# Kernel tuning notes

Hardware: AMD Instinct MI355X
Metric: run time of the kernel (lower is better)

## Reference

```python
import jax, jax.numpy as jnp
import numpy as np

N_SRC = 50000; N_DST = 50000; E = 800000
IN_NODE = 128; IN_EDGE = 16; OUT_NODE = 64; OUT_EDGE = 16; H = 4
LEAKY_SLOPE = 0.01  # F.leaky_relu default used inside dgl EGATConv


def setup_inputs() -> dict:
    key = jax.random.key(0)
    ks = jax.random.split(key, 11)
    return dict(
        nfeats=jax.random.normal(ks[0], (N_SRC, IN_NODE), jnp.float32),
        dst_feats=jax.random.normal(ks[1], (N_DST, IN_NODE), jnp.float32),
        reward=jax.random.uniform(ks[2], (E,), jnp.float32),
        src=jax.random.randint(ks[3], (E,), 0, N_SRC),
        dst=jax.random.randint(ks[4], (E,), 0, N_DST),
        W_ns=jax.random.normal(ks[5], (IN_NODE, H * OUT_NODE), jnp.float32) * 0.05,
        b_ns=jnp.zeros((H * OUT_NODE,), jnp.float32),
        W_ni=jax.random.normal(ks[6], (IN_NODE, H * OUT_EDGE), jnp.float32) * 0.05,
        W_nj=jax.random.normal(ks[7], (IN_NODE, H * OUT_EDGE), jnp.float32) * 0.05,
        W_fij=jax.random.normal(ks[8], (IN_EDGE, H * OUT_EDGE), jnp.float32) * 0.05,
        attn=jax.random.normal(ks[9], (H, OUT_EDGE), jnp.float32) * 0.05,
        b_e=jnp.zeros((H * OUT_EDGE,), jnp.float32),
    )


def reference(nfeats, dst_feats, reward, src, dst,
              W_ns, b_ns, W_ni, W_nj, W_fij, attn, b_e):
    # EGAT.forward with num_layers=1: efeats = reward repeated to IN_EDGE cols
    efeats = jnp.repeat(reward[:, None], IN_EDGE, axis=1)              # (E, Fe_in)
    # --- EGATConv ---
    f_ni = nfeats @ W_ni                                               # (Ns, H*Fe)
    f_nj = dst_feats @ W_nj                                            # (Nd, H*Fe)
    f_out = f_ni[src] + f_nj[dst] + efeats @ W_fij + b_e               # (E, H*Fe)
    f_out = jax.nn.leaky_relu(f_out, LEAKY_SLOPE).reshape(E, H, OUT_EDGE)
    e = jnp.einsum('ehf,hf->eh', f_out, attn)                          # (E, H)
    # edge softmax over incoming edges of each dst node (stable)
    m = jax.ops.segment_max(e, dst, num_segments=N_DST)                # (Nd, H)
    a = jnp.exp(e - m[dst])
    s = jax.ops.segment_sum(a, dst, num_segments=N_DST)                # (Nd, H)
    a = a / jnp.where(s > 0, s, 1.0)[dst]                              # (E, H)
    # weighted aggregation of projected src features
    h_src = (nfeats @ W_ns + b_ns).reshape(N_SRC, H, OUT_NODE)
    msg = h_src[src] * a[:, :, None]                                   # (E, H, Fn)
    h_out = jax.ops.segment_sum(msg, dst, num_segments=N_DST)          # (Nd, H, Fn)
    # wrapper: mean over heads then ReLU
    return jax.nn.relu(h_out.mean(axis=1))                             # (Nd, Fn)
```

## Files before the change

kernel.cpp:

```cpp
#include <hip/hip_runtime.h>

#define IN_NODE 128
#define OUT_NODE 64
#define NHEAD 4
#define HN 256
#define HE 64
#define LEAKY 0.01f

typedef __attribute__((ext_vector_type(8))) short bf16x8;
typedef __attribute__((ext_vector_type(4))) float f32x4;
typedef __attribute__((ext_vector_type(2))) float f32x2;

__device__ __forceinline__ float bf2f(unsigned short u) {
    union { unsigned u; float f; } v; v.u = ((unsigned)u) << 16; return v.f;
}
__device__ __forceinline__ unsigned short f2bf(float x) {
    union { float f; unsigned u; } v; v.f = x;
    unsigned r = v.u + 0x7FFF + ((v.u >> 16) & 1);
    return (unsigned short)(r >> 16);
}
__device__ __forceinline__ bf16x8 cvt8(float4 a, float4 b) {
    bf16x8 r;
    r[0] = (short)f2bf(a.x); r[1] = (short)f2bf(a.y);
    r[2] = (short)f2bf(a.z); r[3] = (short)f2bf(a.w);
    r[4] = (short)f2bf(b.x); r[5] = (short)f2bf(b.y);
    r[6] = (short)f2bf(b.z); r[7] = (short)f2bf(b.w);
    return r;
}
__device__ __forceinline__ f32x2 bfcvt2(unsigned d) {
    union { unsigned u; float f; } lo, hi;
    lo.u = d << 16; hi.u = d & 0xFFFF0000u;
    f32x2 r; r.x = lo.f; r.y = hi.f; return r;
}

__global__ void prep_hist(const float* __restrict__ W_fij,
                          const float* __restrict__ W_ni,
                          const float* __restrict__ W_ns,
                          const float* __restrict__ W_nj,
                          const int* __restrict__ dst,
                          float* __restrict__ wsum, unsigned short* __restrict__ WT,
                          int* __restrict__ cnt, int E) {
    int b = blockIdx.x;
    if (b == 0) {
        int k = threadIdx.x;
        if (k < 64) {
            float s = 0.f;
#pragma unroll
            for (int c = 0; c < 16; ++c) s += W_fij[c * 64 + k];
            wsum[k] = s;
        }
        return;
    }
    if (b <= 12) {
        int base = (b - 1) * 4096 + threadIdx.x;
#pragma unroll
        for (int i = 0; i < 16; ++i) {
            int idx = base + i * 256;
            int g   = idx >> 11;
            int rem = idx & 2047;
            int c   = rem >> 9;
            int l   = (rem >> 3) & 63;
            int j   = rem & 7;
            int nl  = l & 15;
            int k   = c * 32 + (l >> 4) * 8 + j;
            unsigned short v;
            if (g < 4)       v = f2bf(W_ni[k * 64  + g * 16 + nl]);
            else if (g < 20) v = f2bf(W_ns[k * 256 + (g - 4) * 16 + nl]);
            else             v = f2bf(W_nj[k * 64  + (g - 20) * 16 + nl]);
            WT[idx] = v;
        }
        return;
    }
    int i = (b - 13) * 256 + threadIdx.x;
    if (i < E) atomicAdd(&cnt[dst[i]], 1);
}

__global__ __launch_bounds__(256) void scan_all(const int* __restrict__ cnt,
                                                int* __restrict__ row_ptr,
                                                int* __restrict__ partials,
                                                int* __restrict__ flags,
                                                int n, int E, int nb) {
    __shared__ int sums[256];
    __shared__ int s_base;
    int tid = threadIdx.x, b = blockIdx.x;
    int base = b * 1024;
    int v[4]; int tsum = 0;
#pragma unroll
    for (int j = 0; j < 4; ++j) {
        int idx = base + tid * 4 + j;
        v[j] = (idx < n) ? cnt[idx] : 0;
        tsum += v[j];
    }
    sums[tid] = tsum;
    __syncthreads();
    for (int off = 1; off < 256; off <<= 1) {
        int x = (tid >= off) ? sums[tid - off] : 0;
        __syncthreads();
        sums[tid] += x;
        __syncthreads();
    }
    if (tid == 255) {
        __hip_atomic_store(&partials[b], sums[255], __ATOMIC_RELAXED, __HIP_MEMORY_SCOPE_AGENT);
        __hip_atomic_store(&flags[b], 1, __ATOMIC_RELEASE, __HIP_MEMORY_SCOPE_AGENT);
    }
    if (tid < 64) {
        int val = 0;
        if (tid < nb) {
            while (__hip_atomic_load(&flags[tid], __ATOMIC_ACQUIRE, __HIP_MEMORY_SCOPE_AGENT) == 0) {
                __builtin_amdgcn_s_sleep(1);
            }
            val = __hip_atomic_load(&partials[tid], __ATOMIC_RELAXED, __HIP_MEMORY_SCOPE_AGENT);
        }
#pragma unroll
        for (int o = 1; o < 64; o <<= 1) {
            int x = __shfl_up(val, o);
            if (tid >= o) val += x;
        }
        int off = (b > 0) ? __shfl(val, b - 1) : 0;
        if (tid == 0) s_base = off;
    }
    __syncthreads();
    int run = s_base + sums[tid] - tsum;
#pragma unroll
    for (int j = 0; j < 4; ++j) {
        int idx = base + tid * 4 + j;
        if (idx < n) row_ptr[idx] = run;
        run += v[j];
    }
    if (b == nb - 1 && tid == 0) row_ptr[n] = E;
}

template<int NG, int G0>
__device__ __forceinline__ void gemm_tile(
    const float* __restrict__ A, int rowBase, int M,
    const unsigned short* __restrict__ WB, const float* __restrict__ b_ns,
    unsigned short* __restrict__ f_ni, unsigned short* __restrict__ h_src,
    unsigned short* __restrict__ f_nj, unsigned short* As)
{
    const int t = threadIdx.x;
    const float4* A4 = reinterpret_cast<const float4*>(A);
#pragma unroll
    for (int j = 0; j < 4; ++j) {
        int gi = j * 256 + t;
        int r  = gi >> 4;
        int gr = rowBase + r; if (gr >= M) gr = M - 1;
        int fi = (gi & 15) * 2;
        float4 a0 = A4[(size_t)gr * 32 + fi];
        float4 a1 = A4[(size_t)gr * 32 + fi + 1];
        int byteoff = (gi * 16) ^ ((r & 7) << 4);
        *reinterpret_cast<bf16x8*>(reinterpret_cast<char*>(As) + byteoff) = cvt8(a0, a1);
    }
    __syncthreads();

    const int lane = t & 63, w = t >> 6;
    const int rw = rowBase + w * 16;
    if (rw >= M) return;
    const int m = lane & 15, q = lane >> 4;
    const int tr = w * 16 + m;

    f32x4 acc[NG] = {};
    const char* Asb = reinterpret_cast<const char*>(As);
#pragma unroll
    for (int c = 0; c < 4; ++c) {
        int gi  = tr * 16 + c * 4 + q;
        int off = (gi * 16) ^ ((tr & 7) << 4);
        bf16x8 af = *reinterpret_cast<const bf16x8*>(Asb + off);
#pragma unroll
        for (int g = 0; g < NG; ++g) {
            bf16x8 bf = *reinterpret_cast<const bf16x8*>(
                WB + (size_t)(((G0 + g) * 4 + c) * 64 + lane) * 8);
            acc[g] = __builtin_amdgcn_mfma_f32_16x16x32_bf16(af, bf, acc[g], 0, 0, 0);
        }
    }

#pragma unroll
    for (int g = 0; g < NG; ++g) {
        const int ga = G0 + g;
        unsigned short* C; int N, colBase; const float* bias = nullptr;
        if (ga < 4)       { C = f_ni;  N = 64;  colBase = ga * 16; }
        else if (ga < 20) { C = h_src; N = 256; colBase = (ga - 4) * 16; bias = b_ns; }
        else              { C = f_nj;  N = 64;  colBase = (ga - 20) * 16; }
        int col = colBase + m;
        float bv = bias ? bias[col] : 0.f;
#pragma unroll
        for (int rr = 0; rr < 4; ++rr) {
            int orow = rw + q * 4 + rr;
            if (orow < M) C[(size_t)orow * N + col] = f2bf(acc[g][rr] + bv);
        }
    }
}

__global__ __launch_bounds__(256) void mega(
    const float* __restrict__ nfeats, const float* __restrict__ dst_feats,
    const unsigned short* __restrict__ WT, const float* __restrict__ b_ns,
    const int* __restrict__ src, const int* __restrict__ dst,
    const float* __restrict__ reward, const int* __restrict__ row_ptr,
    int* __restrict__ cnt,
    unsigned short* __restrict__ f_ni, unsigned short* __restrict__ h_src,
    unsigned short* __restrict__ f_nj, int2* __restrict__ sr_s,
    int Ns, int Nd, int E, int nBlkNf, int nBlkDj, int nScatter)
{
    __shared__ __align__(16) unsigned short As[64 * 128];
    const int g = blockIdx.x / 3, r = blockIdx.x % 3;
    if (r == 0) {
        if (g < nBlkNf) {
            gemm_tile<20, 0>(nfeats, g * 64, Ns, WT, b_ns, f_ni, h_src, f_nj, As);
        } else if (g < nBlkNf + nBlkDj) {
            gemm_tile<4, 20>(dst_feats, (g - nBlkNf) * 64, Nd, WT, b_ns, f_ni, h_src, f_nj, As);
        }
        return;
    }
    const int sb = g * 2 + (r - 1);
    if (sb >= nScatter) return;
    int i = sb * 256 + threadIdx.x;
    if (i >= E) return;
    int d = dst[i];
    int pos = row_ptr[d] + atomicSub(&cnt[d], 1) - 1;
    sr_s[pos] = make_int2(src[i], __float_as_int(reward[i]));
}

struct G { uint2 ui; uint4 h0; uint4 h1; };
__device__ __forceinline__ G gatherE(const unsigned short* __restrict__ f_ni,
                                     const unsigned short* __restrict__ h_src,
                                     int sn, int ll, int hq) {
    G g;
    g.ui = *reinterpret_cast<const uint2*>(f_ni + (size_t)sn * HE + 4 * ll);
    const unsigned short* hp = h_src + (size_t)sn * HN + hq;
    g.h0 = *reinterpret_cast<const uint4*>(hp);
    g.h1 = *reinterpret_cast<const uint4*>(hp + 8);
    return g;
}

__global__ __launch_bounds__(256) void fused_agg(
    const unsigned short* __restrict__ f_ni, const unsigned short* __restrict__ f_nj,
    const unsigned short* __restrict__ h_src, const int2* __restrict__ sr_s,
    const int* __restrict__ row_ptr,
    const float* __restrict__ wsum, const float* __restrict__ b_e,
    const float* __restrict__ attn, float* __restrict__ out, int Nd)
{
    __shared__ float red[4][1024];
    const int wv = threadIdx.x >> 6, lane = threadIdx.x & 63;
    const int d = blockIdx.x * 4 + wv;
    if (d >= Nd) return;
    const int ll = lane & 15, sub = lane >> 4;
    const int hq = ((lane >> 2) & 3) * 64 + (lane & 3) * 16;
    const int mql = (lane >> 1) & 3;

    float4 wsv = *reinterpret_cast<const float4*>(wsum + 4 * ll);
    float4 bev = *reinterpret_cast<const float4*>(b_e + 4 * ll);
    float4 atv = *reinterpret_cast<const float4*>(attn + 4 * ll);
    f32x2 ws01 = {wsv.x, wsv.y}, ws23 = {wsv.z, wsv.w};
    f32x2 at01 = {atv.x, atv.y}, at23 = {atv.z, atv.w};
    const f32x2 lk2 = {LEAKY, LEAKY};

    const int beg = row_ptr[d];
    const int end = row_ptr[d + 1];
    const int deg = end - beg;

    float den = 0.f;
    f32x2 a0 = {}, a1 = {}, a2 = {}, a3 = {}, a4 = {}, a5 = {}, a6 = {}, a7 = {};

    if (deg > 0) {
        uint2 uj = *reinterpret_cast<const uint2*>(f_nj + (size_t)d * HE + 4 * ll);
        f32x2 bb01 = bfcvt2(uj.x) + (f32x2){bev.x, bev.y};
        f32x2 bb23 = bfcvt2(uj.y) + (f32x2){bev.z, bev.w};
        const int nq = (deg + 3) >> 2;
        const int last = end - 1;

#define LDSR(q) ({ int qq_ = ((q) < nq) ? (q) : (nq - 1);                 \
                   int slot_ = beg + qq_ * 4 + sub;                       \
                   if (slot_ > last) slot_ = last;                        \
                   sr_s[slot_]; })

#define COMPUTE(sr, gg, kq) do {                                          \
    float r_ = __int_as_float((sr).y);                                    \
    f32x2 r2_ = {r_, r_};                                                 \
    f32x2 v01_ = bfcvt2((gg).ui.x) + r2_ * ws01 + bb01;                   \
    f32x2 v23_ = bfcvt2((gg).ui.y) + r2_ * ws23 + bb23;                   \
    v01_ = __builtin_elementwise_max(v01_, v01_ * lk2);                   \
    v23_ = __builtin_elementwise_max(v23_, v23_ * lk2);                   \
    f32x2 t2_ = v01_ * at01 + v23_ * at23;                                \
    float t_ = t2_.x + t2_.y;                                             \
    t_ += __shfl_xor(t_, 1);                                              \
    t_ += __shfl_xor(t_, 2);                                              \
    float ev_ = ((beg + (kq) * 4 + sub) < end) ? __expf(t_) : 0.f;        \
    den += ev_;                                                           \
    f32x2 ev2_ = {ev_, ev_};                                              \
    a0 += bfcvt2((gg).h0.x) * ev2_;                                       \
    a1 += bfcvt2((gg).h0.y) * ev2_;                                       \
    a2 += bfcvt2((gg).h0.z) * ev2_;                                       \
    a3 += bfcvt2((gg).h0.w) * ev2_;                                       \
    a4 += bfcvt2((gg).h1.x) * ev2_;                                       \
    a5 += bfcvt2((gg).h1.y) * ev2_;                                       \
    a6 += bfcvt2((gg).h1.z) * ev2_;                                       \
    a7 += bfcvt2((gg).h1.w) * ev2_;                                       \
} while (0)

        int2 sr0 = LDSR(0), sr1 = LDSR(1);
        G gA = gatherE(f_ni, h_src, sr0.x, ll, hq);
        for (int k = 0; k < nq; ++k) {
            int2 sr2 = LDSR(k + 2);
            G gB = gatherE(f_ni, h_src, sr1.x, ll, hq);
            COMPUTE(sr0, gA, k);
            sr0 = sr1; sr1 = sr2; gA = gB;
        }
#undef COMPUTE
#undef LDSR
    }

    den += __shfl_xor(den, 16);
    den += __shfl_xor(den, 32);
    float sc = (den > 0.f) ? 0.25f / den : 0.f;
    float* wr = &red[wv][lane * 16];
    float4 s0 = {a0.x * sc, a0.y * sc, a1.x * sc, a1.y * sc};
    float4 s1 = {a2.x * sc, a2.y * sc, a3.x * sc, a3.y * sc};
    float4 s2 = {a4.x * sc, a4.y * sc, a5.x * sc, a5.y * sc};
    float4 s3 = {a6.x * sc, a6.y * sc, a7.x * sc, a7.y * sc};
    *reinterpret_cast<float4*>(wr + ((0 ^ mql) << 2)) = s0;
    *reinterpret_cast<float4*>(wr + ((1 ^ mql) << 2)) = s1;
    *reinterpret_cast<float4*>(wr + ((2 ^ mql) << 2)) = s2;
    *reinterpret_cast<float4*>(wr + ((3 ^ mql) << 2)) = s3;
    asm volatile("s_waitcnt lgkmcnt(0)" ::: "memory");
    float ssum = 0.f;
    const int e = lane & 15, c45 = lane >> 4;
#pragma unroll
    for (int s = 0; s < 4; ++s)
#pragma unroll
        for (int h = 0; h < 4; ++h) {
            int L = s * 16 + h * 4 + c45;
            int m2 = (L >> 1) & 3;
            int fi = L * 16 + (((e >> 2) ^ m2) << 2) + (e & 3);
            ssum += red[wv][fi];
        }
    out[(size_t)d * OUT_NODE + lane] = fmaxf(ssum, 0.f);
}

static inline char* align256(char* p) {
    return (char*)(((uintptr_t)p + 255) & ~(uintptr_t)255);
}

extern "C" void kernel_launch(void* const* d_in, const int* in_sizes, int n_in,
                              void* d_out, int out_size, void* d_ws, size_t ws_size,
                              hipStream_t stream) {
    const float* nfeats    = (const float*)d_in[0];
    const float* dst_feats = (const float*)d_in[1];
    const float* reward    = (const float*)d_in[2];
    const int*   src       = (const int*)d_in[3];
    const int*   dst       = (const int*)d_in[4];
    const float* W_ns      = (const float*)d_in[5];
    const float* b_ns      = (const float*)d_in[6];
    const float* W_ni      = (const float*)d_in[7];
    const float* W_nj      = (const float*)d_in[8];
    const float* W_fij     = (const float*)d_in[9];
    const float* attn      = (const float*)d_in[10];
    const float* b_e       = (const float*)d_in[11];
    float* out = (float*)d_out;

    const int Ns = in_sizes[0] / IN_NODE;
    const int Nd = in_sizes[1] / IN_NODE;
    const int E  = in_sizes[2];

    char* ws = (char*)d_ws;
    unsigned short* f_ni  = (unsigned short*)ws; ws = align256(ws + (size_t)Ns * HE * 2);
    unsigned short* f_nj  = (unsigned short*)ws; ws = align256(ws + (size_t)Nd * HE * 2);
    unsigned short* h_src = (unsigned short*)ws; ws = align256(ws + (size_t)Ns * HN * 2);
    unsigned short* WT    = (unsigned short*)ws; ws = align256(ws + 49152 * 2);
    float* wsum    = (float*)ws; ws = align256(ws + HE * 4);
    int*   cnt     = (int*)ws;
    int*   flags   = cnt + Nd;   ws = align256(ws + (size_t)(Nd + 64) * 4);
    int*   row_ptr = (int*)ws;   ws = align256(ws + (size_t)(Nd + 1) * 4);
    int*   partials= (int*)ws;   ws = align256(ws + 256 * 4);
    int2*  sr_s    = (int2*)ws;  ws = align256(ws + (size_t)E * 8);

    hipMemsetAsync(cnt, 0, (size_t)(Nd + 64) * 4, stream);

    prep_hist<<<13 + (E + 255) / 256, 256, 0, stream>>>(
        W_fij, W_ni, W_ns, W_nj, dst, wsum, WT, cnt, E);

    int nb = (Nd + 1023) / 1024;
    scan_all<<<nb, 256, 0, stream>>>(cnt, row_ptr, partials, flags, Nd, E, nb);

    int nBlkNf = (Ns + 63) / 64;
    int nBlkDj = (Nd + 63) / 64;
    int nG = nBlkNf + nBlkDj;
    int nScatter = (E + 255) / 256;
    int nGroups = (nG > (nScatter + 1) / 2) ? nG : (nScatter + 1) / 2;
    mega<<<nGroups * 3, 256, 0, stream>>>(
        nfeats, dst_feats, WT, b_ns, src, dst, reward, row_ptr, cnt,
        f_ni, h_src, f_nj, sr_s, Ns, Nd, E, nBlkNf, nBlkDj, nScatter);

    fused_agg<<<(Nd + 3) / 4, 256, 0, stream>>>(
        f_ni, f_nj, h_src, sr_s, row_ptr, wsum, b_e, attn, out, Nd);
}
```

Baseline: 273.0 us.

## Record atomic ranks in histogram, split node GEMM tiles, deepen gather prefetch

```diff
diff --git a/kernel.cpp b/kernel.cpp
--- a/kernel.cpp
+++ b/kernel.cpp
@@ -39,7 +39,7 @@
                           const float* __restrict__ W_nj,
                           const int* __restrict__ dst,
                           float* __restrict__ wsum, unsigned short* __restrict__ WT,
-                          int* __restrict__ cnt, int E) {
+                          int* __restrict__ cnt, int* __restrict__ rank, int E) {
     int b = blockIdx.x;
     if (b == 0) {
         int k = threadIdx.x;
@@ -72,7 +72,7 @@
         return;
     }
     int i = (b - 13) * 256 + threadIdx.x;
-    if (i < E) atomicAdd(&cnt[dst[i]], 1);
+    if (i < E) rank[i] = atomicAdd(&cnt[dst[i]], 1);
 }
 
 __global__ __launch_bounds__(256) void scan_all(const int* __restrict__ cnt,
@@ -195,7 +195,7 @@
     const unsigned short* __restrict__ WT, const float* __restrict__ b_ns,
     const int* __restrict__ src, const int* __restrict__ dst,
     const float* __restrict__ reward, const int* __restrict__ row_ptr,
-    int* __restrict__ cnt,
+    const int* __restrict__ rank,
     unsigned short* __restrict__ f_ni, unsigned short* __restrict__ h_src,
     unsigned short* __restrict__ f_nj, int2* __restrict__ sr_s,
     int Ns, int Nd, int E, int nBlkNf, int nBlkDj, int nScatter)
@@ -203,10 +203,14 @@
     __shared__ __align__(16) unsigned short As[64 * 128];
     const int g = blockIdx.x / 3, r = blockIdx.x % 3;
     if (r == 0) {
-        if (g < nBlkNf) {
-            gemm_tile<20, 0>(nfeats, g * 64, Ns, WT, b_ns, f_ni, h_src, f_nj, As);
-        } else if (g < nBlkNf + nBlkDj) {
-            gemm_tile<4, 20>(dst_feats, (g - nBlkNf) * 64, Nd, WT, b_ns, f_ni, h_src, f_nj, As);
+        if (g < 2 * nBlkNf) {
+            int tile = g >> 1;
+            if ((g & 1) == 0)
+                gemm_tile<10, 0>(nfeats, tile * 64, Ns, WT, b_ns, f_ni, h_src, f_nj, As);
+            else
+                gemm_tile<10, 10>(nfeats, tile * 64, Ns, WT, b_ns, f_ni, h_src, f_nj, As);
+        } else if (g < 2 * nBlkNf + nBlkDj) {
+            gemm_tile<4, 20>(dst_feats, (g - 2 * nBlkNf) * 64, Nd, WT, b_ns, f_ni, h_src, f_nj, As);
         }
         return;
     }
@@ -215,7 +219,7 @@
     int i = sb * 256 + threadIdx.x;
     if (i >= E) return;
     int d = dst[i];
-    int pos = row_ptr[d] + atomicSub(&cnt[d], 1) - 1;
+    int pos = row_ptr[d] + rank[i];
     sr_s[pos] = make_int2(src[i], __float_as_int(reward[i]));
 }
 
@@ -296,13 +300,17 @@
     a7 += bfcvt2((gg).h1.w) * ev2_;                                       \
 } while (0)
 
-        int2 sr0 = LDSR(0), sr1 = LDSR(1);
+        int2 sr0 = LDSR(0), sr1 = LDSR(1), sr2 = LDSR(2);
         G gA = gatherE(f_ni, h_src, sr0.x, ll, hq);
-        for (int k = 0; k < nq; ++k) {
-            int2 sr2 = LDSR(k + 2);
-            G gB = gatherE(f_ni, h_src, sr1.x, ll, hq);
+        G gB = gatherE(f_ni, h_src, sr1.x, ll, hq);
+        for (int k = 0; k < nq; k += 2) {
+            int2 sr3 = LDSR(k + 3);
+            G gC = gatherE(f_ni, h_src, sr2.x, ll, hq);
             COMPUTE(sr0, gA, k);
-            sr0 = sr1; sr1 = sr2; gA = gB;
+            int2 sr4 = LDSR(k + 4);
+            G gD = gatherE(f_ni, h_src, sr3.x, ll, hq);
+            if (k + 1 < nq) COMPUTE(sr1, gB, k + 1);
+            sr0 = sr2; sr1 = sr3; sr2 = sr4; gA = gC; gB = gD;
         }
 #undef COMPUTE
 #undef LDSR
@@ -371,22 +379,23 @@
     int*   row_ptr = (int*)ws;   ws = align256(ws + (size_t)(Nd + 1) * 4);
     int*   partials= (int*)ws;   ws = align256(ws + 256 * 4);
     int2*  sr_s    = (int2*)ws;  ws = align256(ws + (size_t)E * 8);
+    int*   rank    = (int*)ws;   ws = align256(ws + (size_t)E * 4);
 
     hipMemsetAsync(cnt, 0, (size_t)(Nd + 64) * 4, stream);
 
     prep_hist<<<13 + (E + 255) / 256, 256, 0, stream>>>(
-        W_fij, W_ni, W_ns, W_nj, dst, wsum, WT, cnt, E);
+        W_fij, W_ni, W_ns, W_nj, dst, wsum, WT, cnt, rank, E);
 
     int nb = (Nd + 1023) / 1024;
     scan_all<<<nb, 256, 0, stream>>>(cnt, row_ptr, partials, flags, Nd, E, nb);
 
     int nBlkNf = (Ns + 63) / 64;
     int nBlkDj = (Nd + 63) / 64;
-    int nG = nBlkNf + nBlkDj;
+    int nG = 2 * nBlkNf + nBlkDj;
     int nScatter = (E + 255) / 256;
     int nGroups = (nG > (nScatter + 1) / 2) ? nG : (nScatter + 1) / 2;
     mega<<<nGroups * 3, 256, 0, stream>>>(
-        nfeats, dst_feats, WT, b_ns, src, dst, reward, row_ptr, cnt,
+        nfeats, dst_feats, WT, b_ns, src, dst, reward, row_ptr, rank,
         f_ni, h_src, f_nj, sr_s, Ns, Nd, E, nBlkNf, nBlkDj, nScatter);
 
     fused_agg<<<(Nd + 3) / 4, 256, 0, stream>>>(
```

Measured after the change: 262.6 us. -3.8%, faster.
